# Performance work log

Measured on AMD Instinct MI355X. Metric: run time of the kernel, lower is better.

The kernel has to match this reference:

```python
import jax, jax.numpy as jnp
import numpy as np

EPS = 1e-16  # epsilon used in cosine similarity and sharpen normalization


def _address(memory, key_vector, key_strength, gate, shift_weights, sharpen, prev_w):
    # --- content addressing: eq. 5-6 (cosine similarity + strength-scaled softmax) ---
    k = key_vector[:, None, :]                                   # (B,1,M)
    dot = jnp.sum(memory * k, axis=-1)                           # (B,N)
    denom = jnp.linalg.norm(memory, axis=-1) * jnp.linalg.norm(k, axis=-1)
    sim = dot / jnp.maximum(denom, EPS)                          # cosine similarity (B,N)
    wc = jax.nn.softmax(key_strength * sim, axis=1)              # (B,N)
    # --- interpolation: eq. 7 ---
    wg = gate * wc + (1.0 - gate) * prev_w                       # (B,N)
    # --- circular shift (eq. 8), vectorized over batch via rolls ---
    K = shift_weights.shape[1]
    pad = K // 2
    # correlate with wrap padding: out[i] = sum_j s[j] * w[(i + j - pad) mod N]
    ws = sum(shift_weights[:, j:j + 1] * jnp.roll(wg, pad - j, axis=1) for j in range(K))
    # --- sharpen: eq. 9 ---
    w = ws ** sharpen
    w = w / (jnp.sum(w, axis=1, keepdims=True) + EPS)
    return w


def reference(memory, key_vector, key_strength, interp_gate_scalar, shift_weights,
              sharpen_scalar, previous_weights, erase_vector, add_vector):
    w = _address(memory, key_vector, key_strength, interp_gate_scalar,
                 shift_weights, sharpen_scalar, previous_weights)      # (B,N)
    # read (section 3.1): r = w @ M
    read = jnp.matmul(w[:, None, :], memory)[:, 0, :]                  # (B,M)
    # write (section 3.2) -- faithful to the source, which uses M * (1 - erase + add)
    erase = w[:, :, None] * erase_vector[:, None, :]                   # (B,N,M)
    add = w[:, :, None] * add_vector[:, None, :]                       # (B,N,M)
    new_memory = memory * (1.0 - erase + add)                          # (B,N,M)
    return read, new_memory, w


def setup_inputs() -> dict:
    B, N, M = 64, 16384, 64
    key = jax.random.key(0)
    ks = jax.random.split(key, 9)
    memory = jax.random.uniform(ks[0], (B, N, M), dtype=jnp.float32)          # uniform init as in module
    key_vector = jax.random.normal(ks[1], (B, M), dtype=jnp.float32)
    key_strength = jax.random.uniform(ks[2], (B, 1), dtype=jnp.float32)       # beta in (0,1)
    interp_gate = jax.random.uniform(ks[3], (B, 1), dtype=jnp.float32)        # g in (0,1)
    shift_w = jax.random.uniform(ks[4], (B, 3), dtype=jnp.float32)
    shift_w = shift_w / jnp.sum(shift_w, axis=1, keepdims=True)               # shift distribution
    sharpen = 1.0 + 2.0 * jax.random.uniform(ks[5], (B, 1), dtype=jnp.float32)  # gamma >= 1
    prev_w = jax.random.uniform(ks[6], (B, N), dtype=jnp.float32)
    prev_w = prev_w / jnp.sum(prev_w, axis=1, keepdims=True)                  # valid weighting
    erase_v = jax.random.uniform(ks[7], (B, M), dtype=jnp.float32)            # e in (0,1)
    add_v = jax.random.uniform(ks[8], (B, M), dtype=jnp.float32)
    return {
        'memory': memory,
        'key_vector': key_vector,
        'key_strength': key_strength,
        'interp_gate_scalar': interp_gate,
        'shift_weights': shift_w,
        'sharpen_scalar': sharpen,
        'previous_weights': prev_w,
        'erase_vector': erase_v,
        'add_vector': add_v,
    }
```

## Files before the change

### kernel.cpp

```cpp
#include <hip/hip_runtime.h>
#include <math.h>

#define EPSF 1e-16f
constexpr int B = 64, N = 16384, M = 64;
constexpr int ROWS_PER_BLOCK = 64;

typedef float vf4 __attribute__((ext_vector_type(4)));

__device__ __forceinline__ float red16(float v) {
    v += __shfl_xor(v, 1);
    v += __shfl_xor(v, 2);
    v += __shfl_xor(v, 4);
    v += __shfl_xor(v, 8);
    return v;
}
__device__ __forceinline__ float red64(float v) {
    v += __shfl_xor(v, 1);
    v += __shfl_xor(v, 2);
    v += __shfl_xor(v, 4);
    v += __shfl_xor(v, 8);
    v += __shfl_xor(v, 16);
    v += __shfl_xor(v, 32);
    return v;
}

__global__ __launch_bounds__(256) void k1_sim(const float* __restrict__ mem,
                                              const float* __restrict__ key,
                                              const float* __restrict__ beta,
                                              float* __restrict__ e_out,
                                              float* __restrict__ sum_e) {
    const int b    = blockIdx.y;
    const int tid  = threadIdx.x;
    const int wave = tid >> 6;
    const int lane = tid & 63;
    const int sub  = lane >> 4;
    const int q    = lane & 15;

    const float4 k4 = ((const float4*)(key + b * M))[q];
    float kk = k4.x * k4.x + k4.y * k4.y + k4.z * k4.z + k4.w * k4.w;
    kk = red16(kk);
    const float knorm = sqrtf(kk);
    const float bet = beta[b];

    float local = 0.f;
    const int row0 = blockIdx.x * ROWS_PER_BLOCK;
#pragma unroll
    for (int it = 0; it < 4; ++it) {
        const int row = row0 + it * 16 + wave * 4 + sub;
        const float4 m4 = ((const float4*)(mem + ((size_t)b * N + row) * M))[q];
        float d  = m4.x * k4.x + m4.y * k4.y + m4.z * k4.z + m4.w * k4.w;
        float nn = m4.x * m4.x + m4.y * m4.y + m4.z * m4.z + m4.w * m4.w;
        d  = red16(d);
        nn = red16(nn);
        const float sim = d / fmaxf(sqrtf(nn) * knorm, EPSF);
        const float e = expf(bet * sim);
        if (q == 0) {
            e_out[(size_t)b * N + row] = e;
            local += e;
        }
    }
    local = red64(local);
    __shared__ float lds[4];
    if (lane == 0) lds[wave] = local;
    __syncthreads();
    if (tid == 0) atomicAdd(&sum_e[b], lds[0] + lds[1] + lds[2] + lds[3]);
}

__global__ __launch_bounds__(256) void k2_shift(const float* __restrict__ e_in,
                                                const float* __restrict__ prev_w,
                                                const float* __restrict__ gate,
                                                const float* __restrict__ shiftw,
                                                const float* __restrict__ sharpen,
                                                const float* __restrict__ sum_e,
                                                float* __restrict__ wpow,
                                                float* __restrict__ sum_pow) {
    const int idx = blockIdx.x * 256 + threadIdx.x;
    const int b = idx >> 14;
    const int n = idx & (N - 1);
    const float inv = 1.f / sum_e[b];
    const float g   = gate[b];
    const float s0 = shiftw[b * 3 + 0];
    const float s1 = shiftw[b * 3 + 1];
    const float s2 = shiftw[b * 3 + 2];
    const float sh = sharpen[b];
    const size_t base = (size_t)b * N;
    const int nm = (n - 1) & (N - 1);
    const int np = (n + 1) & (N - 1);
    const float gi = g * inv, om = 1.f - g;
    const float wgm = gi * e_in[base + nm] + om * prev_w[base + nm];
    const float wg0 = gi * e_in[base + n ] + om * prev_w[base + n ];
    const float wgp = gi * e_in[base + np] + om * prev_w[base + np];
    const float wsv = s0 * wgm + s1 * wg0 + s2 * wgp;
    const float wp = powf(wsv, sh);
    wpow[idx] = wp;

    float v = red64(wp);
    __shared__ float lds[4];
    if ((threadIdx.x & 63) == 0) lds[threadIdx.x >> 6] = v;
    __syncthreads();
    if (threadIdx.x == 0) atomicAdd(&sum_pow[b], lds[0] + lds[1] + lds[2] + lds[3]);
}

__global__ __launch_bounds__(256) void k3_update(const float* __restrict__ mem,
                                                 const float* __restrict__ erase,
                                                 const float* __restrict__ addv,
                                                 const float* __restrict__ wpow,
                                                 const float* __restrict__ sum_pow,
                                                 float* __restrict__ read_out,
                                                 float* __restrict__ new_mem,
                                                 float* __restrict__ w_out) {
    const int b    = (B - 1) - blockIdx.y;
    const int tid  = threadIdx.x;
    const int wave = tid >> 6;
    const int lane = tid & 63;
    const int sub  = lane >> 4;
    const int q    = lane & 15;

    const float inv = 1.f / (sum_pow[b] + EPSF);
    const float4 e4 = ((const float4*)(erase + b * M))[q];
    const float4 a4 = ((const float4*)(addv  + b * M))[q];
    const float4 d4 = make_float4(a4.x - e4.x, a4.y - e4.y, a4.z - e4.z, a4.w - e4.w);

    float4 racc = make_float4(0.f, 0.f, 0.f, 0.f);
    const int row0 = N - ROWS_PER_BLOCK - blockIdx.x * ROWS_PER_BLOCK;
#pragma unroll
    for (int it = 3; it >= 0; --it) {
        const int row = row0 + it * 16 + wave * 4 + sub;
        const size_t roff = ((size_t)b * N + row) * M;
        const float w = wpow[(size_t)b * N + row] * inv;
        const vf4 m4 = __builtin_nontemporal_load((const vf4*)(mem + roff) + q);
        vf4 nm4;
        nm4.x = m4.x * (1.f + w * d4.x);
        nm4.y = m4.y * (1.f + w * d4.y);
        nm4.z = m4.z * (1.f + w * d4.z);
        nm4.w = m4.w * (1.f + w * d4.w);
        __builtin_nontemporal_store(nm4, (vf4*)(new_mem + roff) + q);
        racc.x += w * m4.x;
        racc.y += w * m4.y;
        racc.z += w * m4.z;
        racc.w += w * m4.w;
        if (q == 0) w_out[(size_t)b * N + row] = w;
    }
#pragma unroll
    for (int m = 16; m <= 32; m <<= 1) {
        racc.x += __shfl_xor(racc.x, m);
        racc.y += __shfl_xor(racc.y, m);
        racc.z += __shfl_xor(racc.z, m);
        racc.w += __shfl_xor(racc.w, m);
    }
    __shared__ float lds[4][64];
    if (sub == 0) {
        lds[wave][q * 4 + 0] = racc.x;
        lds[wave][q * 4 + 1] = racc.y;
        lds[wave][q * 4 + 2] = racc.z;
        lds[wave][q * 4 + 3] = racc.w;
    }
    __syncthreads();
    if (wave == 0) {
        const float s = lds[0][lane] + lds[1][lane] + lds[2][lane] + lds[3][lane];
        atomicAdd(&read_out[b * M + lane], s);
    }
}

extern "C" void kernel_launch(void* const* d_in, const int* in_sizes, int n_in,
                              void* d_out, int out_size, void* d_ws, size_t ws_size,
                              hipStream_t stream) {
    const float* mem     = (const float*)d_in[0];
    const float* key     = (const float*)d_in[1];
    const float* beta    = (const float*)d_in[2];
    const float* gate    = (const float*)d_in[3];
    const float* shiftw  = (const float*)d_in[4];
    const float* sharpen = (const float*)d_in[5];
    const float* prev_w  = (const float*)d_in[6];
    const float* erase   = (const float*)d_in[7];
    const float* addv    = (const float*)d_in[8];

    float* out      = (float*)d_out;
    float* read_out = out;
    float* new_mem  = out + B * M;
    float* w_out    = out + B * M + (size_t)B * N * M;

    float* ws      = (float*)d_ws;
    float* sum_e   = ws;
    float* sum_pow = ws + 64;
    float* wpow    = ws + 128;

    float* e_buf = w_out;

    hipMemsetAsync(sum_e, 0, 2 * 64 * sizeof(float), stream);
    hipMemsetAsync(read_out, 0, B * M * sizeof(float), stream);

    dim3 grid1(N / ROWS_PER_BLOCK, B);
    k1_sim<<<grid1, 256, 0, stream>>>(mem, key, beta, e_buf, sum_e);
    k2_shift<<<(B * N) / 256, 256, 0, stream>>>(e_buf, prev_w, gate, shiftw, sharpen,
                                                sum_e, wpow, sum_pow);
    k3_update<<<grid1, 256, 0, stream>>>(mem, erase, addv, wpow, sum_pow,
                                         read_out, new_mem, w_out);
}
```

Baseline: 581.8 us.

## Fuse three NTM kernels into one cooperative kernel with grid syncs

Replaces the three launches (similarity, shift/sharpen, memory update) with a single cooperative kernel of 1024 blocks. Each block owns a contiguous segment of 1024 rows of one batch and keeps the exp values and sharpened weights in LDS, with halo rows recomputed at the edges. Two grid-wide syncs handle the softmax and sharpen normalisations. This removes the intermediate global buffers and launch gaps. It relies on all 1024 blocks being co-resident, and the grid syncs and the reduced parallelism per batch may add latency. The old path remains as a fallback if the cooperative launch fails.

Measured after the change: 724.1 us. +24.5%, slower.

```diff
diff --git a/kernel.cpp b/kernel.cpp
--- a/kernel.cpp
+++ b/kernel.cpp
@@ -1,11 +1,16 @@
 #include <hip/hip_runtime.h>
+#include <hip/hip_cooperative_groups.h>
 #include <math.h>
 
 #define EPSF 1e-16f
 constexpr int B = 64, N = 16384, M = 64;
 constexpr int ROWS_PER_BLOCK = 64;
+constexpr int NBLK = 1024;
+constexpr int SEGS_PER_B = NBLK / B;
+constexpr int ROWS = N / SEGS_PER_B;
 
 typedef float vf4 __attribute__((ext_vector_type(4)));
+namespace cg = cooperative_groups;
 
 __device__ __forceinline__ float red16(float v) {
     v += __shfl_xor(v, 1);
@@ -22,6 +27,147 @@
     v += __shfl_xor(v, 16);
     v += __shfl_xor(v, 32);
     return v;
+}
+
+__global__ __launch_bounds__(256, 4) void fused_ntm(
+    const float* __restrict__ mem, const float* __restrict__ key,
+    const float* __restrict__ beta, const float* __restrict__ gate,
+    const float* __restrict__ shiftw, const float* __restrict__ sharpen,
+    const float* __restrict__ prev_w, const float* __restrict__ erase,
+    const float* __restrict__ addv,
+    float* __restrict__ sum_e, float* __restrict__ sum_pow,
+    float* __restrict__ read_out, float* __restrict__ new_mem,
+    float* __restrict__ w_out)
+{
+    __shared__ float e_s[ROWS + 2];
+    __shared__ float wp_s[ROWS];
+    __shared__ float red_s[4];
+    __shared__ float bsum[4][64];
+    __shared__ float scal[2];
+
+    const int blk  = blockIdx.x;
+    const int b    = blk >> 4;
+    const int seg  = blk & (SEGS_PER_B - 1);
+    const int n0   = seg * ROWS;
+    const int tid  = threadIdx.x;
+    const int wave = tid >> 6;
+    const int lane = tid & 63;
+    const int sub  = lane >> 4;
+    const int q    = lane & 15;
+    const size_t bbase = (size_t)b * N;
+
+    const float4 k4 = ((const float4*)(key + b * M))[q];
+    float kk = k4.x * k4.x + k4.y * k4.y + k4.z * k4.z + k4.w * k4.w;
+    kk = red16(kk);
+    const float knorm = sqrtf(kk);
+    const float bet = beta[b];
+
+    float local = 0.f;
+#pragma unroll 4
+    for (int it = 0; it < ROWS / 16; ++it) {
+        const int r = it * 16 + wave * 4 + sub;
+        const float4 m4 = ((const float4*)(mem + (bbase + n0 + r) * M))[q];
+        float d  = m4.x * k4.x + m4.y * k4.y + m4.z * k4.z + m4.w * k4.w;
+        float nn = m4.x * m4.x + m4.y * m4.y + m4.z * m4.z + m4.w * m4.w;
+        d  = red16(d);
+        nn = red16(nn);
+        const float e = expf(bet * (d / fmaxf(sqrtf(nn) * knorm, EPSF)));
+        if (q == 0) { e_s[1 + r] = e; local += e; }
+    }
+    if (wave < 2 && sub == 0) {
+        const int g = (wave == 0) ? ((n0 - 1) & (N - 1)) : ((n0 + ROWS) & (N - 1));
+        const float4 m4 = ((const float4*)(mem + (bbase + g) * M))[q];
+        float d  = m4.x * k4.x + m4.y * k4.y + m4.z * k4.z + m4.w * k4.w;
+        float nn = m4.x * m4.x + m4.y * m4.y + m4.z * m4.z + m4.w * m4.w;
+        d  = red16(d);
+        nn = red16(nn);
+        const float e = expf(bet * (d / fmaxf(sqrtf(nn) * knorm, EPSF)));
+        if (q == 0) e_s[(wave == 0) ? 0 : ROWS + 1] = e;
+    }
+    local = red64(local);
+    if (lane == 0) red_s[wave] = local;
+    __syncthreads();
+    if (tid == 0) atomicAdd(&sum_e[b], red_s[0] + red_s[1] + red_s[2] + red_s[3]);
+
+    cg::this_grid().sync();
+
+    if (tid == 0)
+        scal[0] = __hip_atomic_load(&sum_e[b], __ATOMIC_RELAXED, __HIP_MEMORY_SCOPE_AGENT);
+    __syncthreads();
+    const float inv_e = 1.f / scal[0];
+    const float gt = gate[b];
+    const float s0 = shiftw[b * 3 + 0];
+    const float s1 = shiftw[b * 3 + 1];
+    const float s2 = shiftw[b * 3 + 2];
+    const float sh = sharpen[b];
+    const float gi = gt * inv_e, om = 1.f - gt;
+    float psum = 0.f;
+#pragma unroll
+    for (int j = 0; j < ROWS / 256; ++j) {
+        const int r  = j * 256 + tid;
+        const int gl = n0 + r;
+        const int nm = (gl - 1) & (N - 1);
+        const int np = (gl + 1) & (N - 1);
+        const float wgm = gi * e_s[r]     + om * prev_w[bbase + nm];
+        const float wg0 = gi * e_s[r + 1] + om * prev_w[bbase + gl];
+        const float wgp = gi * e_s[r + 2] + om * prev_w[bbase + np];
+        const float wsv = s0 * wgm + s1 * wg0 + s2 * wgp;
+        const float wp = powf(wsv, sh);
+        wp_s[r] = wp;
+        psum += wp;
+    }
+    psum = red64(psum);
+    if (lane == 0) red_s[wave] = psum;
+    __syncthreads();
+    if (tid == 0) atomicAdd(&sum_pow[b], red_s[0] + red_s[1] + red_s[2] + red_s[3]);
+
+    cg::this_grid().sync();
+
+    if (tid == 0)
+        scal[1] = __hip_atomic_load(&sum_pow[b], __ATOMIC_RELAXED, __HIP_MEMORY_SCOPE_AGENT);
+    __syncthreads();
+    const float inv = 1.f / (scal[1] + EPSF);
+    const float4 e4 = ((const float4*)(erase + b * M))[q];
+    const float4 a4 = ((const float4*)(addv  + b * M))[q];
+    const float4 d4 = make_float4(a4.x - e4.x, a4.y - e4.y, a4.z - e4.z, a4.w - e4.w);
+
+    float4 racc = make_float4(0.f, 0.f, 0.f, 0.f);
+#pragma unroll 4
+    for (int it = ROWS / 16 - 1; it >= 0; --it) {
+        const int r = it * 16 + wave * 4 + sub;
+        const size_t roff = (bbase + n0 + r) * M;
+        const float w = wp_s[r] * inv;
+        const vf4 m4 = __builtin_nontemporal_load((const vf4*)(mem + roff) + q);
+        vf4 nm4;
+        nm4.x = m4.x * (1.f + w * d4.x);
+        nm4.y = m4.y * (1.f + w * d4.y);
+        nm4.z = m4.z * (1.f + w * d4.z);
+        nm4.w = m4.w * (1.f + w * d4.w);
+        __builtin_nontemporal_store(nm4, (vf4*)(new_mem + roff) + q);
+        racc.x += w * m4.x;
+        racc.y += w * m4.y;
+        racc.z += w * m4.z;
+        racc.w += w * m4.w;
+        if (q == 0) w_out[bbase + n0 + r] = w;
+    }
+#pragma unroll
+    for (int mm = 16; mm <= 32; mm <<= 1) {
+        racc.x += __shfl_xor(racc.x, mm);
+        racc.y += __shfl_xor(racc.y, mm);
+        racc.z += __shfl_xor(racc.z, mm);
+        racc.w += __shfl_xor(racc.w, mm);
+    }
+    if (sub == 0) {
+        bsum[wave][q * 4 + 0] = racc.x;
+        bsum[wave][q * 4 + 1] = racc.y;
+        bsum[wave][q * 4 + 2] = racc.z;
+        bsum[wave][q * 4 + 3] = racc.w;
+    }
+    __syncthreads();
+    if (wave == 0) {
+        const float s = bsum[0][lane] + bsum[1][lane] + bsum[2][lane] + bsum[3][lane];
+        atomicAdd(&read_out[b * M + lane], s);
+    }
 }
 
 __global__ __launch_bounds__(256) void k1_sim(const float* __restrict__ mem,
@@ -185,15 +331,22 @@
     float* sum_pow = ws + 64;
     float* wpow    = ws + 128;
 
-    float* e_buf = w_out;
-
     hipMemsetAsync(sum_e, 0, 2 * 64 * sizeof(float), stream);
     hipMemsetAsync(read_out, 0, B * M * sizeof(float), stream);
 
-    dim3 grid1(N / ROWS_PER_BLOCK, B);
-    k1_sim<<<grid1, 256, 0, stream>>>(mem, key, beta, e_buf, sum_e);
-    k2_shift<<<(B * N) / 256, 256, 0, stream>>>(e_buf, prev_w, gate, shiftw, sharpen,
-                                                sum_e, wpow, sum_pow);
-    k3_update<<<grid1, 256, 0, stream>>>(mem, erase, addv, wpow, sum_pow,
-                                         read_out, new_mem, w_out);
-}
+    void* args[] = {(void*)&mem, (void*)&key, (void*)&beta, (void*)&gate,
+                    (void*)&shiftw, (void*)&sharpen, (void*)&prev_w, (void*)&erase,
+                    (void*)&addv, (void*)&sum_e, (void*)&sum_pow,
+                    (void*)&read_out, (void*)&new_mem, (void*)&w_out};
+    hipError_t err = hipLaunchCooperativeKernel((const void*)fused_ntm, dim3(NBLK),
+                                                dim3(256), args, 0, stream);
+    if (err != hipSuccess) {
+        float* e_buf = w_out;
+        dim3 grid1(N / ROWS_PER_BLOCK, B);
+        k1_sim<<<grid1, 256, 0, stream>>>(mem, key, beta, e_buf, sum_e);
+        k2_shift<<<(B * N) / 256, 256, 0, stream>>>(e_buf, prev_w, gate, shiftw,
+                                                    sharpen, sum_e, wpow, sum_pow);
+        k3_update<<<grid1, 256, 0, stream>>>(mem, erase, addv, wpow, sum_pow,
+                                             read_out, new_mem, w_out);
+    }
+}
```
